# Performance work log

Hardware: AMD Instinct MI355X
Metric: run time of the kernel (lower is better)

Reference implementation:

```python
import jax, jax.numpy as jnp
import numpy as np

# config (from init_kwargs)
VOCAB = 32000
EMBED_DIM = 2048
ATO = 32000            # added_tokens_offset
SCO = 1000             # sin_cos_numbers_offset
VQ_START = 33100       # vqgan_start_index
VQ_END = 49484         # vqgan_end_index
VQ_VOCAB = 16384
VQ_DIM = 256
IMG_OFFSET = 33100     # image_token_offset
ADDED_SIZE = IMG_OFFSET - ATO - SCO  # 100


def sin_cos_table(num_positions, embedding_dim):
    position = np.arange(num_positions)[:, np.newaxis]
    dim = np.arange(embedding_dim)[np.newaxis, :]
    angle_rates = 1 / np.power(10000, 2 * (dim // 2) / np.float32(embedding_dim))
    pe = np.zeros((num_positions, embedding_dim), dtype=np.float32)
    pe[:, 0::2] = np.sin(position * angle_rates[:, 0::2])
    pe[:, 1::2] = np.cos(position * angle_rates[:, 1::2])
    return pe


def setup_inputs() -> dict:
    key = jax.random.key(0)
    k1, k2, k3, k4, k5 = jax.random.split(key, 5)
    B, S = 4, 8192
    x = jax.random.randint(k1, (B, S), 0, VQ_END, dtype=jnp.int32)
    token_emb = jax.random.normal(k2, (VOCAB, EMBED_DIM), dtype=jnp.float32) * 0.02
    added_emb = jax.random.normal(k3, (ADDED_SIZE, EMBED_DIM), dtype=jnp.float32) * 0.02
    numbers_emb = jnp.asarray(sin_cos_table(SCO, EMBED_DIM))  # frozen sin-cos
    codebook = jax.random.normal(k4, (VQ_VOCAB, VQ_DIM), dtype=jnp.float32) * 0.02  # frozen VQGAN codebook
    proj_w = jax.random.normal(k5, (EMBED_DIM, VQ_DIM), dtype=jnp.float32) * 0.02   # Linear(vq_dim->embed_dim, bias=False)
    return {"x": x, "token_emb": token_emb, "added_emb": added_emb,
            "numbers_emb": numbers_emb, "codebook": codebook, "proj_w": proj_w}


def reference(x, token_emb, added_emb, numbers_emb, codebook, proj_w):
    # mutually exclusive range masks over the token-id space
    text_mask = (x >= 0) & (x < ATO)
    number_mask = (x >= ATO) & (x < ATO + SCO)
    three_d_mask = (x >= ATO + SCO) & (x < VQ_START)
    image_mask = (x >= VQ_START) & (x < VQ_END)

    # index arithmetic; masked-out positions clamp to 0 (matches torch clamping)
    text_idx = jnp.where(text_mask, x, 0)
    num_idx = jnp.where(number_mask, x - ATO, 0)
    td_idx = jnp.where(three_d_mask, x - ATO - SCO, 0)
    img_idx = jnp.where(image_mask, x - IMG_OFFSET, 0)

    text_e = token_emb[text_idx]                       # [B,S,D]
    num_e = numbers_emb[num_idx]                       # [B,S,D]
    td_e = added_emb[td_idx]                           # [B,S,D]
    img_e = jnp.einsum('bsv,dv->bsd', codebook[img_idx], proj_w)  # gather + proj

    sel = lambda m, e: jnp.where(m[..., None], e, jnp.zeros((), e.dtype))
    # masks are disjoint, so summing masked contributions == scatter-write
    return sel(text_mask, text_e) + sel(number_mask, num_e) + sel(three_d_mask, td_e) + sel(image_mask, img_e)
```

## Files before the change

### kernel.cpp

```cpp
#include <hip/hip_runtime.h>
#include <stdint.h>

#define ATO 32000
#define SCO 1000
#define VQ_START 33100
#define VQ_END 49484
#define EMB_D 2048
#define VQ_K 256
#define NSPLIT 8
#define NCOLS_PER_BLOCK (EMB_D / NSPLIT)

typedef __bf16 bf16_t;
typedef bf16_t bf16x8 __attribute__((ext_vector_type(8)));
typedef float floatx4 __attribute__((ext_vector_type(4)));
typedef float f32x4v __attribute__((ext_vector_type(4)));

__global__ void zero_count_kernel(int* __restrict__ c) {
    if (threadIdx.x == 0) *c = 0;
}

__global__ __launch_bounds__(256, 8) void gather_compact_kernel(
    const int* __restrict__ x,
    const float* __restrict__ token_emb,
    const float* __restrict__ added_emb,
    const float* __restrict__ numbers_emb,
    float* __restrict__ out,
    int* __restrict__ img_count,
    unsigned int* __restrict__ img_list,
    int n_tok)
{
    const int wave = threadIdx.x >> 6;
    const int lane = threadIdx.x & 63;
    const int t = blockIdx.x * 4 + wave;
    if (t >= n_tok) return;

    const int v = x[t];
    const float* src = nullptr;
    if (v >= 0 && v < ATO) {
        src = token_emb + (size_t)v * EMB_D;
    } else if (v >= ATO && v < ATO + SCO) {
        src = numbers_emb + (size_t)(v - ATO) * EMB_D;
    } else if (v >= ATO + SCO && v < VQ_START) {
        src = added_emb + (size_t)(v - ATO - SCO) * EMB_D;
    } else if (v >= VQ_START && v < VQ_END) {
        if (lane == 0) {
            const int slot = atomicAdd(img_count, 1);
            img_list[slot] = (unsigned int)t | ((unsigned int)(v - VQ_START) << 18);
        }
        return;
    }

    f32x4v* d4 = (f32x4v*)(out + (size_t)t * EMB_D);
    if (src) {
        const f32x4v* s4 = (const f32x4v*)src;
        f32x4v r[8];
#pragma unroll
        for (int j = 0; j < 8; ++j) r[j] = s4[lane + 64 * j];
#pragma unroll
        for (int j = 0; j < 8; ++j)
            __builtin_nontemporal_store(r[j], &d4[lane + 64 * j]);
    } else {
        const f32x4v z = {0.f, 0.f, 0.f, 0.f};
#pragma unroll
        for (int j = 0; j < 8; ++j)
            __builtin_nontemporal_store(z, &d4[lane + 64 * j]);
    }
}

__global__ __launch_bounds__(256, 1) void img_proj_kernel(
    const float* __restrict__ codebook,
    const float* __restrict__ proj_w,
    float* __restrict__ out,
    const int* __restrict__ img_count,
    const unsigned int* __restrict__ img_list)
{
    __shared__ bf16_t w_hi[64 * 32 * 8];
    __shared__ bf16_t w_lo[64 * 32 * 8];
    __shared__ unsigned int toks[64];

    const int count  = *img_count;
    const int m_base = blockIdx.x * 64;
    if (m_base >= count) return;

    const int tid    = threadIdx.x;
    const int lane   = tid & 63;
    const int wave   = tid >> 6;
    const int wave_m = wave >> 1;
    const int wave_n = wave & 1;
    const int l15    = lane & 15;
    const int quad   = lane >> 4;
    const int nc0    = blockIdx.y * NCOLS_PER_BLOCK;

    if (tid < 64) {
        int mg = m_base + tid;
        if (mg >= count) mg = count - 1;
        toks[tid] = img_list[mg];
    }
    __syncthreads();

    bf16x8 a_hi[2][8], a_lo[2][8];
#pragma unroll
    for (int msub = 0; msub < 2; ++msub) {
        const unsigned int pk = toks[wave_m * 32 + msub * 16 + l15];
        const int row = (int)(pk >> 18);
        const float* arow = codebook + (size_t)row * VQ_K;
#pragma unroll
        for (int kk = 0; kk < 8; ++kk) {
            const float4* p = (const float4*)(arow + kk * 32 + quad * 8);
            const float4 f0 = p[0];
            const float4 f1 = p[1];
            const float f[8] = {f0.x, f0.y, f0.z, f0.w, f1.x, f1.y, f1.z, f1.w};
            bf16x8 h, l;
#pragma unroll
            for (int j = 0; j < 8; ++j) {
                const bf16_t hb = (bf16_t)f[j];
                h[j] = hb;
                l[j] = (bf16_t)(f[j] - (float)hb);
            }
            a_hi[msub][kk] = h;
            a_lo[msub][kk] = l;
        }
    }

    const floatx4 vzero = {0.f, 0.f, 0.f, 0.f};

    for (int nc = nc0; nc < nc0 + NCOLS_PER_BLOCK; nc += 64) {
        __syncthreads();
#pragma unroll
        for (int it = 0; it < 8; ++it) {
            const int i = tid + it * 256;
            const int n = i >> 5;
            const int g = i & 31;
            const float4* p = (const float4*)(proj_w + (size_t)(nc + n) * VQ_K + g * 8);
            const float4 f0 = p[0];
            const float4 f1 = p[1];
            const float f[8] = {f0.x, f0.y, f0.z, f0.w, f1.x, f1.y, f1.z, f1.w};
            bf16x8 h, l;
#pragma unroll
            for (int j = 0; j < 8; ++j) {
                const bf16_t hb = (bf16_t)f[j];
                h[j] = hb;
                l[j] = (bf16_t)(f[j] - (float)hb);
            }
            const int off = (n * 32 + (g ^ (n & 31))) * 8;
            *(bf16x8*)(w_hi + off) = h;
            *(bf16x8*)(w_lo + off) = l;
        }
        __syncthreads();

        floatx4 acc[2][2];
#pragma unroll
        for (int i = 0; i < 2; ++i)
#pragma unroll
            for (int j = 0; j < 2; ++j) acc[i][j] = vzero;

#pragma unroll
        for (int kk = 0; kk < 8; ++kk) {
#pragma unroll
            for (int nsub = 0; nsub < 2; ++nsub) {
                const int n_l = wave_n * 32 + nsub * 16 + l15;
                const int g   = kk * 4 + quad;
                const int off = (n_l * 32 + (g ^ (n_l & 31))) * 8;
                const bf16x8 bh = *(const bf16x8*)(w_hi + off);
                const bf16x8 bl = *(const bf16x8*)(w_lo + off);
#pragma unroll
                for (int msub = 0; msub < 2; ++msub) {
                    acc[msub][nsub] = __builtin_amdgcn_mfma_f32_16x16x32_bf16(
                        a_lo[msub][kk], bh, acc[msub][nsub], 0, 0, 0);
                    acc[msub][nsub] = __builtin_amdgcn_mfma_f32_16x16x32_bf16(
                        a_hi[msub][kk], bl, acc[msub][nsub], 0, 0, 0);
                    acc[msub][nsub] = __builtin_amdgcn_mfma_f32_16x16x32_bf16(
                        a_hi[msub][kk], bh, acc[msub][nsub], 0, 0, 0);
                }
            }
        }

#pragma unroll
        for (int msub = 0; msub < 2; ++msub) {
#pragma unroll
            for (int nsub = 0; nsub < 2; ++nsub) {
#pragma unroll
                for (int r = 0; r < 4; ++r) {
                    const int m_local = wave_m * 32 + msub * 16 + quad * 4 + r;
                    if (m_base + m_local < count) {
                        const int tok = (int)(toks[m_local] & 0x3FFFFu);
                        const int col = nc + wave_n * 32 + nsub * 16 + l15;
                        out[(size_t)tok * EMB_D + col] = acc[msub][nsub][r];
                    }
                }
            }
        }
    }
}

__global__ __launch_bounds__(256, 4) void fused_fallback_kernel(
    const int* __restrict__ x,
    const float* __restrict__ token_emb,
    const float* __restrict__ added_emb,
    const float* __restrict__ numbers_emb,
    const float* __restrict__ codebook,
    const float* __restrict__ proj_w,
    float* __restrict__ out)
{
    const int t = blockIdx.x;
    const int v = x[t];
    float* orow = out + (size_t)t * EMB_D;

    if (v >= VQ_START && v < VQ_END) {
        __shared__ float cb[VQ_K];
        cb[threadIdx.x] = codebook[(size_t)(v - VQ_START) * VQ_K + threadIdx.x];
        __syncthreads();
#pragma unroll
        for (int j = 0; j < 8; ++j) {
            const int n = threadIdx.x + 256 * j;
            const float* wrow = proj_w + (size_t)n * VQ_K;
            float s = 0.f;
#pragma unroll 4
            for (int k = 0; k < VQ_K; k += 4) {
                const float4 w4 = *(const float4*)(wrow + k);
                s += w4.x * cb[k] + w4.y * cb[k + 1] + w4.z * cb[k + 2] + w4.w * cb[k + 3];
            }
            orow[n] = s;
        }
        return;
    }

    const float* src = nullptr;
    if (v >= 0 && v < ATO)                  src = token_emb + (size_t)v * EMB_D;
    else if (v >= ATO && v < ATO + SCO)     src = numbers_emb + (size_t)(v - ATO) * EMB_D;
    else if (v >= ATO + SCO && v < VQ_START) src = added_emb + (size_t)(v - ATO - SCO) * EMB_D;

    float4* d4 = (float4*)orow;
    if (src) {
        const float4* s4 = (const float4*)src;
        d4[threadIdx.x]       = s4[threadIdx.x];
        d4[threadIdx.x + 256] = s4[threadIdx.x + 256];
    } else {
        const float4 z = make_float4(0.f, 0.f, 0.f, 0.f);
        d4[threadIdx.x]       = z;
        d4[threadIdx.x + 256] = z;
    }
}

extern "C" void kernel_launch(void* const* d_in, const int* in_sizes, int n_in,
                              void* d_out, int out_size, void* d_ws, size_t ws_size,
                              hipStream_t stream) {
    const int*   x           = (const int*)d_in[0];
    const float* token_emb   = (const float*)d_in[1];
    const float* added_emb   = (const float*)d_in[2];
    const float* numbers_emb = (const float*)d_in[3];
    const float* codebook    = (const float*)d_in[4];
    const float* proj_w      = (const float*)d_in[5];
    float*       out         = (float*)d_out;

    const int n_tok = in_sizes[0];

    const size_t ws_needed = 16 + (size_t)n_tok * sizeof(unsigned int);
    if (d_ws == nullptr || ws_size < ws_needed) {
        fused_fallback_kernel<<<n_tok, 256, 0, stream>>>(
            x, token_emb, added_emb, numbers_emb, codebook, proj_w, out);
        return;
    }

    int* img_count         = (int*)d_ws;
    unsigned int* img_list = (unsigned int*)((char*)d_ws + 16);

    zero_count_kernel<<<1, 64, 0, stream>>>(img_count);

    const int gather_blocks = (n_tok + 3) / 4;
    gather_compact_kernel<<<gather_blocks, 256, 0, stream>>>(
        x, token_emb, added_emb, numbers_emb, out, img_count, img_list, n_tok);

    const int gemm_blocks_m = (n_tok + 63) / 64;
    dim3 gemm_grid(gemm_blocks_m, NSPLIT);
    img_proj_kernel<<<gemm_grid, 256, 0, stream>>>(
        codebook, proj_w, out, img_count, img_list);
}
```

Baseline: 569.8 us.

## Pre-split codebook/proj to bf16 hi/lo and fuse gather with image GEMM

Adds a prep kernel that compacts image tokens with a wave-level ballot and a single atomic per wave, and converts the full codebook and projection weights to bf16 hi/lo arrays in workspace. The gather/copy work and the image projection GEMM now run in one launch over a shared 1D grid, so copy blocks can overlap with GEMM blocks. This removes the per-block repeated fp32-to-bf16 splitting and one kernel boundary. In exchange it converts the whole 16384-row codebook every call even though only gathered rows are needed, and it requires a larger workspace.

```diff
diff --git a/kernel.cpp b/kernel.cpp
--- a/kernel.cpp
+++ b/kernel.cpp
@@ -7,6 +7,7 @@
 #define VQ_END 49484
 #define EMB_D 2048
 #define VQ_K 256
+#define VQ_VOCAB 16384
 #define NSPLIT 8
 #define NCOLS_PER_BLOCK (EMB_D / NSPLIT)
 
@@ -19,77 +20,124 @@
     if (threadIdx.x == 0) *c = 0;
 }
 
-__global__ __launch_bounds__(256, 8) void gather_compact_kernel(
+#define PREP_COMPACT_BLOCKS 128
+#define PREP_CONV_CB 2048
+#define PREP_CONV_PW 256
+
+__global__ __launch_bounds__(256) void prep_kernel(
+    const int* __restrict__ x, int n_tok,
+    int* __restrict__ img_count, unsigned int* __restrict__ img_list,
+    const float* __restrict__ codebook, const float* __restrict__ proj_w,
+    bf16_t* __restrict__ cb_hi, bf16_t* __restrict__ cb_lo,
+    bf16_t* __restrict__ pw_hi, bf16_t* __restrict__ pw_lo)
+{
+    const int b = blockIdx.x;
+    if (b < PREP_COMPACT_BLOCKS) {
+        const int t = b * 256 + threadIdx.x;
+        int v = 0;
+        bool is_img = false;
+        if (t < n_tok) {
+            v = x[t];
+            is_img = (v >= VQ_START) && (v < VQ_END);
+        }
+        const unsigned long long m = __ballot(is_img);
+        const int lane = threadIdx.x & 63;
+        int base = 0;
+        if (lane == 0 && m) base = atomicAdd(img_count, __popcll(m));
+        base = __shfl(base, 0);
+        if (is_img) {
+            const int below = __popcll(m & ((1ull << lane) - 1ull));
+            img_list[base + below] =
+                (unsigned int)t | ((unsigned int)(v - VQ_START) << 18);
+        }
+        return;
+    }
+
+    const int cbb = b - PREP_COMPACT_BLOCKS;
+    const float* src;
+    bf16_t* dh;
+    bf16_t* dl;
+    size_t base_e;
+    if (cbb < PREP_CONV_CB) {
+        src = codebook; dh = cb_hi; dl = cb_lo;
+        base_e = (size_t)cbb * 2048;
+    } else {
+        src = proj_w; dh = pw_hi; dl = pw_lo;
+        base_e = (size_t)(cbb - PREP_CONV_CB) * 2048;
+    }
+    const size_t e = base_e + (size_t)threadIdx.x * 8;
+    const float4 f0 = *(const float4*)(src + e);
+    const float4 f1 = *(const float4*)(src + e + 4);
+    const float f[8] = {f0.x, f0.y, f0.z, f0.w, f1.x, f1.y, f1.z, f1.w};
+    bf16x8 h, l;
+#pragma unroll
+    for (int j = 0; j < 8; ++j) {
+        const bf16_t hb = (bf16_t)f[j];
+        h[j] = hb;
+        l[j] = (bf16_t)(f[j] - (float)hb);
+    }
+    *(bf16x8*)(dh + e) = h;
+    *(bf16x8*)(dl + e) = l;
+}
+
+__global__ __launch_bounds__(256, 2) void mega_kernel(
     const int* __restrict__ x,
     const float* __restrict__ token_emb,
     const float* __restrict__ added_emb,
     const float* __restrict__ numbers_emb,
-    float* __restrict__ out,
-    int* __restrict__ img_count,
-    unsigned int* __restrict__ img_list,
-    int n_tok)
-{
-    const int wave = threadIdx.x >> 6;
-    const int lane = threadIdx.x & 63;
-    const int t = blockIdx.x * 4 + wave;
-    if (t >= n_tok) return;
-
-    const int v = x[t];
-    const float* src = nullptr;
-    if (v >= 0 && v < ATO) {
-        src = token_emb + (size_t)v * EMB_D;
-    } else if (v >= ATO && v < ATO + SCO) {
-        src = numbers_emb + (size_t)(v - ATO) * EMB_D;
-    } else if (v >= ATO + SCO && v < VQ_START) {
-        src = added_emb + (size_t)(v - ATO - SCO) * EMB_D;
-    } else if (v >= VQ_START && v < VQ_END) {
-        if (lane == 0) {
-            const int slot = atomicAdd(img_count, 1);
-            img_list[slot] = (unsigned int)t | ((unsigned int)(v - VQ_START) << 18);
-        }
-        return;
-    }
-
-    f32x4v* d4 = (f32x4v*)(out + (size_t)t * EMB_D);
-    if (src) {
-        const f32x4v* s4 = (const f32x4v*)src;
-        f32x4v r[8];
-#pragma unroll
-        for (int j = 0; j < 8; ++j) r[j] = s4[lane + 64 * j];
-#pragma unroll
-        for (int j = 0; j < 8; ++j)
-            __builtin_nontemporal_store(r[j], &d4[lane + 64 * j]);
-    } else {
-        const f32x4v z = {0.f, 0.f, 0.f, 0.f};
-#pragma unroll
-        for (int j = 0; j < 8; ++j)
-            __builtin_nontemporal_store(z, &d4[lane + 64 * j]);
-    }
-}
-
-__global__ __launch_bounds__(256, 1) void img_proj_kernel(
-    const float* __restrict__ codebook,
-    const float* __restrict__ proj_w,
+    const bf16_t* __restrict__ cb_hi, const bf16_t* __restrict__ cb_lo,
+    const bf16_t* __restrict__ pw_hi, const bf16_t* __restrict__ pw_lo,
     float* __restrict__ out,
     const int* __restrict__ img_count,
-    const unsigned int* __restrict__ img_list)
+    const unsigned int* __restrict__ img_list,
+    int n_tok, int gemm_total)
 {
     __shared__ bf16_t w_hi[64 * 32 * 8];
     __shared__ bf16_t w_lo[64 * 32 * 8];
     __shared__ unsigned int toks[64];
 
+    const int tid  = threadIdx.x;
+    const int lane = tid & 63;
+    const int wave = tid >> 6;
+
+    if (blockIdx.x >= gemm_total) {
+        const int t = (blockIdx.x - gemm_total) * 4 + wave;
+        if (t >= n_tok) return;
+        const int v = x[t];
+        if (v >= VQ_START && v < VQ_END) return;
+
+        const float* src = nullptr;
+        if (v >= 0 && v < ATO)                   src = token_emb + (size_t)v * EMB_D;
+        else if (v >= ATO && v < ATO + SCO)      src = numbers_emb + (size_t)(v - ATO) * EMB_D;
+        else if (v >= ATO + SCO && v < VQ_START) src = added_emb + (size_t)(v - ATO - SCO) * EMB_D;
+
+        f32x4v* d4 = (f32x4v*)(out + (size_t)t * EMB_D);
+        if (src) {
+            const f32x4v* s4 = (const f32x4v*)src;
+            f32x4v r[8];
+#pragma unroll
+            for (int j = 0; j < 8; ++j) r[j] = s4[lane + 64 * j];
+#pragma unroll
+            for (int j = 0; j < 8; ++j)
+                __builtin_nontemporal_store(r[j], &d4[lane + 64 * j]);
+        } else {
+            const f32x4v z = {0.f, 0.f, 0.f, 0.f};
+#pragma unroll
+            for (int j = 0; j < 8; ++j)
+                __builtin_nontemporal_store(z, &d4[lane + 64 * j]);
+        }
+        return;
+    }
+
     const int count  = *img_count;
-    const int m_base = blockIdx.x * 64;
+    const int m_base = (blockIdx.x >> 3) * 64;
     if (m_base >= count) return;
 
-    const int tid    = threadIdx.x;
-    const int lane   = tid & 63;
-    const int wave   = tid >> 6;
     const int wave_m = wave >> 1;
     const int wave_n = wave & 1;
     const int l15    = lane & 15;
     const int quad   = lane >> 4;
-    const int nc0    = blockIdx.y * NCOLS_PER_BLOCK;
+    const int nc0    = (blockIdx.x & 7) * NCOLS_PER_BLOCK;
 
     if (tid < 64) {
         int mg = m_base + tid;
@@ -103,22 +151,12 @@
     for (int msub = 0; msub < 2; ++msub) {
         const unsigned int pk = toks[wave_m * 32 + msub * 16 + l15];
         const int row = (int)(pk >> 18);
-        const float* arow = codebook + (size_t)row * VQ_K;
+        const bf16_t* ah = cb_hi + (size_t)row * VQ_K;
+        const bf16_t* al = cb_lo + (size_t)row * VQ_K;
 #pragma unroll
         for (int kk = 0; kk < 8; ++kk) {
-            const float4* p = (const float4*)(arow + kk * 32 + quad * 8);
-            const float4 f0 = p[0];
-            const float4 f1 = p[1];
-            const float f[8] = {f0.x, f0.y, f0.z, f0.w, f1.x, f1.y, f1.z, f1.w};
-            bf16x8 h, l;
-#pragma unroll
-            for (int j = 0; j < 8; ++j) {
-                const bf16_t hb = (bf16_t)f[j];
-                h[j] = hb;
-                l[j] = (bf16_t)(f[j] - (float)hb);
-            }
-            a_hi[msub][kk] = h;
-            a_lo[msub][kk] = l;
+            a_hi[msub][kk] = *(const bf16x8*)(ah + kk * 32 + quad * 8);
+            a_lo[msub][kk] = *(const bf16x8*)(al + kk * 32 + quad * 8);
         }
     }
 
@@ -131,17 +169,9 @@
             const int i = tid + it * 256;
             const int n = i >> 5;
             const int g = i & 31;
-            const float4* p = (const float4*)(proj_w + (size_t)(nc + n) * VQ_K + g * 8);
-            const float4 f0 = p[0];
-            const float4 f1 = p[1];
-            const float f[8] = {f0.x, f0.y, f0.z, f0.w, f1.x, f1.y, f1.z, f1.w};
-            bf16x8 h, l;
-#pragma unroll
-            for (int j = 0; j < 8; ++j) {
-                const bf16_t hb = (bf16_t)f[j];
-                h[j] = hb;
-                l[j] = (bf16_t)(f[j] - (float)hb);
-            }
+            const size_t ge = (size_t)(nc + n) * VQ_K + g * 8;
+            const bf16x8 h = *(const bf16x8*)(pw_hi + ge);
+            const bf16x8 l = *(const bf16x8*)(pw_lo + ge);
             const int off = (n * 32 + (g ^ (n & 31))) * 8;
             *(bf16x8*)(w_hi + off) = h;
             *(bf16x8*)(w_lo + off) = l;
@@ -255,7 +285,12 @@
 
     const int n_tok = in_sizes[0];
 
-    const size_t ws_needed = 16 + (size_t)n_tok * sizeof(unsigned int);
+    const size_t list_bytes = (size_t)n_tok * sizeof(unsigned int);
+    const size_t conv_off   = (16 + list_bytes + 63) & ~(size_t)63;
+    const size_t cb_bytes   = (size_t)VQ_VOCAB * VQ_K * sizeof(bf16_t);
+    const size_t pw_bytes   = (size_t)EMB_D * VQ_K * sizeof(bf16_t);
+    const size_t ws_needed  = conv_off + 2 * cb_bytes + 2 * pw_bytes;
+
     if (d_ws == nullptr || ws_size < ws_needed) {
         fused_fallback_kernel<<<n_tok, 256, 0, stream>>>(
             x, token_emb, added_emb, numbers_emb, codebook, proj_w, out);
@@ -264,15 +299,21 @@
 
     int* img_count         = (int*)d_ws;
     unsigned int* img_list = (unsigned int*)((char*)d_ws + 16);
+    bf16_t* cb_hi = (bf16_t*)((char*)d_ws + conv_off);
+    bf16_t* cb_lo = (bf16_t*)((char*)d_ws + conv_off + cb_bytes);
+    bf16_t* pw_hi = (bf16_t*)((char*)d_ws + conv_off + 2 * cb_bytes);
+    bf16_t* pw_lo = (bf16_t*)((char*)d_ws + conv_off + 2 * cb_bytes + pw_bytes);
 
     zero_count_kernel<<<1, 64, 0, stream>>>(img_count);
 
-    const int gather_blocks = (n_tok + 3) / 4;
-    gather_compact_kernel<<<gather_blocks, 256, 0, stream>>>(
-        x, token_emb, added_emb, numbers_emb, out, img_count, img_list, n_tok);
-
-    const int gemm_blocks_m = (n_tok + 63) / 64;
-    dim3 gemm_grid(gemm_blocks_m, NSPLIT);
-    img_proj_kernel<<<gemm_grid, 256, 0, stream>>>(
-        codebook, proj_w, out, img_count, img_list);
-}
+    prep_kernel<<<PREP_COMPACT_BLOCKS + PREP_CONV_CB + PREP_CONV_PW, 256, 0, stream>>>(
+        x, n_tok, img_count, img_list, codebook, proj_w, cb_hi, cb_lo, pw_hi, pw_lo);
+
+    const int gemm_m     = (n_tok + 63) / 64;
+    const int gemm_total = gemm_m * NSPLIT;
+    const int copy_blocks = (n_tok + 3) / 4;
+    mega_kernel<<<gemm_total + copy_blocks, 256, 0, stream>>>(
+        x, token_emb, added_emb, numbers_emb,
+        cb_hi, cb_lo, pw_hi, pw_lo,
+        out, img_count, img_list, n_tok, gemm_total);
+}
```

New measurement: 498.1 us. 12.6% less time.
